# Kernel optimization log

Measured on AMD Instinct MI355X. Metric: run time of the kernel, lower is better.

## Reference

```python
import jax, jax.numpy as jnp
import numpy as np

DIM = 1024
HEADS = 16
HEAD_DIM = DIM // HEADS
SCALE = DIM ** (-0.5)  # NOTE: module scales by full dim, not head dim


def setup_inputs() -> dict:
    key = jax.random.key(0)
    k1, k2, k3, k4 = jax.random.split(key, 4)
    x = jax.random.normal(k1, (4, 2048, DIM), dtype=jnp.float32)
    w_qkv = jax.random.normal(k2, (DIM, 3 * DIM), dtype=jnp.float32) * (DIM ** -0.5)
    w_out = jax.random.normal(k3, (DIM, DIM), dtype=jnp.float32) * (DIM ** -0.5)
    b_out = jax.random.normal(k4, (DIM,), dtype=jnp.float32) * 0.01
    return {"x": x, "w_qkv": w_qkv, "w_out": w_out, "b_out": b_out}


def reference(x, w_qkv, w_out, b_out):
    b, n, _ = x.shape
    qkv = x @ w_qkv  # [b, n, 3*dim]
    # 'b n (qkv h d) -> qkv b h n d'
    qkv = qkv.reshape(b, n, 3, HEADS, HEAD_DIM).transpose(2, 0, 3, 1, 4)
    q, k, v = qkv[0], qkv[1], qkv[2]  # each [b, h, n, d]
    dots = jnp.einsum('bhid,bhjd->bhij', q, k) * SCALE
    attn = jax.nn.softmax(dots, axis=-1)
    out = jnp.einsum('bhij,bhjd->bhid', attn, v)
    out = out.transpose(0, 2, 1, 3).reshape(b, n, DIM)  # 'b h n d -> b n (h d)'
    return out @ w_out + b_out
```

## Files before the change

### kernel.cpp

```cpp
#include <hip/hip_runtime.h>
#include <math.h>

#define BATCH 4
#define SEQ   2048
#define DMODEL 1024
#define HEADS 16
#define DHEAD 64
#define SCALE 0.03125f
#define KEXP  0.045084220027780106f
#define QKV_ELEMS (BATCH * HEADS * SEQ * DHEAD)

typedef __attribute__((ext_vector_type(8))) short short8;
typedef __attribute__((ext_vector_type(4))) float floatx4;
typedef unsigned int u32;

__device__ __forceinline__ unsigned short f2bf(float f) {
  union { float f; unsigned u; } v;
  v.f = f;
  return (unsigned short)((v.u + 0x7FFFu + ((v.u >> 16) & 1u)) >> 16);
}

__device__ __forceinline__ float fast_exp2(float x) {
#if __has_builtin(__builtin_amdgcn_exp2f)
  return __builtin_amdgcn_exp2f(x);
#else
  return __expf(x * 0.6931471805599453f);
#endif
}

__device__ __forceinline__ u32 pack_bf16(float p0, float p1) {
#if __has_builtin(__builtin_amdgcn_cvt_pk_bf16_f32)
  typedef __bf16 bf16x2 __attribute__((ext_vector_type(2)));
  bf16x2 t = __builtin_amdgcn_cvt_pk_bf16_f32(p0, p1);
  u32 r;
  __builtin_memcpy(&r, &t, 4);
  return r;
#else
  u32 a0 = __float_as_uint(p0) + 0x8000u;
  u32 a1 = __float_as_uint(p1) + 0x8000u;
  return __builtin_amdgcn_perm(a1, a0, 0x07060302);
#endif
}

__device__ __forceinline__ void async_ld16(const void* g, void* l) {
  __builtin_amdgcn_global_load_lds(
      (const __attribute__((address_space(1))) u32*)g,
      (__attribute__((address_space(3))) u32*)l, 16, 0, 0);
}

__device__ __forceinline__ void trans_tile(const float* __restrict__ W,
                                           unsigned short* __restrict__ WT,
                                           int K, int N, int n0, int k0,
                                           float (*tile)[33]) {
  const int tx = threadIdx.x & 31, ty = threadIdx.x >> 5;
#pragma unroll
  for (int i = 0; i < 4; ++i)
    tile[ty + i * 8][tx] = W[(size_t)(k0 + ty + i * 8) * N + n0 + tx];
  __syncthreads();
#pragma unroll
  for (int i = 0; i < 4; ++i)
    WT[(size_t)(n0 + ty + i * 8) * K + k0 + tx] = f2bf(tile[tx][ty + i * 8]);
}

__global__ __launch_bounds__(256) void prep_kernel(
    const float* __restrict__ x, const float* __restrict__ wqkv,
    const float* __restrict__ wout, unsigned short* __restrict__ xb,
    unsigned short* __restrict__ wqkvT, unsigned short* __restrict__ woutT) {
  __shared__ float tile[32][33];
  const int bx = blockIdx.x;
  if (bx < 8192) {
    size_t i = ((size_t)bx * 256 + threadIdx.x) * 4;
    float4 v = *(const float4*)(x + i);
    ushort4 o;
    o.x = f2bf(v.x); o.y = f2bf(v.y); o.z = f2bf(v.z); o.w = f2bf(v.w);
    *(ushort4*)(xb + i) = o;
  } else if (bx < 11264) {
    int t = bx - 8192;
    trans_tile(wqkv, wqkvT, 1024, 3072, (t % 96) * 32, (t / 96) * 32, tile);
  } else {
    int t = bx - 11264;
    trans_tile(wout, woutT, 1024, 1024, (t % 32) * 32, (t / 32) * 32, tile);
  }
}

__device__ __forceinline__ void gemm_core(
    const unsigned short* __restrict__ A, const unsigned short* __restrict__ BT,
    unsigned short* As, unsigned short* Bs, int m0, int n0,
    floatx4 acc[4][4]) {
  const int tid = threadIdx.x;
  const int wave = tid >> 6, lane = tid & 63;
  const int quad = lane >> 4, l16 = lane & 15;
  const int wm = wave >> 1, wn = wave & 1;
  const int lrow = lane >> 3, ls = lane & 7;
  const int dblk = ls ^ (lrow & 7);
  const int sw = l16 & 7;

#pragma unroll
  for (int mt = 0; mt < 4; ++mt)
#pragma unroll
    for (int nt = 0; nt < 4; ++nt) acc[mt][nt] = (floatx4){0.f, 0.f, 0.f, 0.f};

  for (int k0 = 0; k0 < DMODEL; k0 += 64) {
    __syncthreads();
#pragma unroll
    for (int i = 0; i < 4; ++i) {
      int chunk = wave * 4 + i;
      int row = chunk * 8 + lrow;
      async_ld16(A + (size_t)(m0 + row) * DMODEL + k0 + dblk * 8,
                 As + chunk * 512);
      async_ld16(BT + (size_t)(n0 + row) * DMODEL + k0 + dblk * 8,
                 Bs + chunk * 512);
    }
    __syncthreads();
#pragma unroll
    for (int kk = 0; kk < 64; kk += 32) {
      const int kb = kk >> 3;
      short8 a[4], b[4];
#pragma unroll
      for (int t = 0; t < 4; ++t) {
        int row = wm * 64 + t * 16 + l16;
        a[t] = *(short8*)(As + row * 64 + (((kb + quad) ^ sw) * 8));
        int rowb = wn * 64 + t * 16 + l16;
        b[t] = *(short8*)(Bs + rowb * 64 + (((kb + quad) ^ sw) * 8));
      }
#pragma unroll
      for (int mt = 0; mt < 4; ++mt)
#pragma unroll
        for (int nt = 0; nt < 4; ++nt)
          acc[mt][nt] = __builtin_amdgcn_mfma_f32_16x16x32_bf16(
              a[mt], b[nt], acc[mt][nt], 0, 0, 0);
    }
  }
}

__global__ __launch_bounds__(256) void gemm_qkv_kernel(
    const unsigned short* __restrict__ A, const unsigned short* __restrict__ BT,
    unsigned short* __restrict__ qk, unsigned short* __restrict__ vtg) {
  __shared__ __align__(16) unsigned char smem[128 * 136 * 2];
  unsigned short* As = (unsigned short*)smem;
  unsigned short* Bs = As + 128 * 64;
  unsigned short* T = (unsigned short*)smem;
  const int tid = threadIdx.x;
  const int wave = tid >> 6, lane = tid & 63;
  const int quad = lane >> 4, l16 = lane & 15;
  const int wm = wave >> 1, wn = wave & 1;
  const int m0 = blockIdx.y * 128, n0 = blockIdx.x * 128;
  floatx4 acc[4][4];
  gemm_core(A, BT, As, Bs, m0, n0, acc);

  const int b = m0 >> 11, ntok = m0 & 2047;
  __syncthreads();

  if (blockIdx.x < 16) {
    const float qsc = (blockIdx.x < 8) ? KEXP : 1.0f;
#pragma unroll
    for (int mt = 0; mt < 4; ++mt) {
#pragma unroll
      for (int nt = 0; nt < 4; ++nt) {
        int c = wn * 64 + nt * 16 + l16;
#pragma unroll
        for (int r = 0; r < 4; ++r) {
          int mloc = wm * 64 + mt * 16 + quad * 4 + r;
          T[mloc * 132 + c] = f2bf(acc[mt][nt][r] * qsc);
        }
      }
    }
    __syncthreads();
    const int which = blockIdx.x >> 3;
    const int h0 = (n0 >> 6) & 15;
    const int inner = tid & 7;
#pragma unroll
    for (int pass = 0; pass < 8; ++pass) {
      int row = pass * 32 + (tid >> 3);
      int token = row >> 1, hh = row & 1;
      *(short8*)(qk + (size_t)which * QKV_ELEMS +
                 (((size_t)((b * HEADS + h0 + hh) * SEQ + ntok + token)) << 6) +
                 inner * 8) = *(short8*)&T[token * 132 + hh * 64 + inner * 8];
    }
  } else {
#pragma unroll
    for (int mt = 0; mt < 4; ++mt) {
#pragma unroll
      for (int nt = 0; nt < 4; ++nt) {
        int c = wn * 64 + nt * 16 + l16;
#pragma unroll
        for (int r = 0; r < 4; ++r) {
          int mloc = wm * 64 + mt * 16 + quad * 4 + r;
          int pcm = (mloc & ~31) | ((mloc & 15) << 1) | ((mloc >> 4) & 1);
          T[c * 136 + pcm] = f2bf(acc[mt][nt][r]);
        }
      }
    }
    __syncthreads();
    const int c = tid >> 1, hh = tid & 1;
    const int nc = n0 - 2048 + c;
    const int h = nc >> 6, d = nc & 63;
    const size_t dstbase =
        (((size_t)(b * HEADS + h)) * DHEAD + d) * SEQ + ntok;
#pragma unroll
    for (int j = 0; j < 8; ++j) {
      int t0 = (2 * j + hh) * 8;
      *(short8*)(vtg + dstbase + t0) = *(short8*)&T[c * 136 + t0];
    }
  }
}

__global__ __launch_bounds__(256) void gemm_out_kernel(
    const unsigned short* __restrict__ A, const unsigned short* __restrict__ BT,
    const float* __restrict__ bias, float* __restrict__ C) {
  __shared__ __align__(16) unsigned short As[128 * 64];
  __shared__ __align__(16) unsigned short Bs[128 * 64];
  const int tid = threadIdx.x;
  const int wave = tid >> 6, lane = tid & 63;
  const int quad = lane >> 4, l16 = lane & 15;
  const int wm = wave >> 1, wn = wave & 1;
  const int m0 = blockIdx.y * 128, n0 = blockIdx.x * 128;
  floatx4 acc[4][4];
  gemm_core(A, BT, As, Bs, m0, n0, acc);

#pragma unroll
  for (int mt = 0; mt < 4; ++mt) {
#pragma unroll
    for (int nt = 0; nt < 4; ++nt) {
      int nc = n0 + wn * 64 + nt * 16 + l16;
      float bv = bias[nc];
#pragma unroll
      for (int r = 0; r < 4; ++r) {
        int m = m0 + wm * 64 + mt * 16 + quad * 4 + r;
        C[(size_t)m * DMODEL + nc] = acc[mt][nt][r] + bv;
      }
    }
  }
}

__global__ __launch_bounds__(256, 4) void attn_kernel(
    const unsigned short* __restrict__ Qb, const unsigned short* __restrict__ Kb,
    const unsigned short* __restrict__ Vtg, unsigned short* __restrict__ Op) {
  __shared__ __align__(16) unsigned short Ks[2][64 * 64];
  __shared__ __align__(16) unsigned short Vs[2][64 * 64];
  __shared__ __align__(16) unsigned short Pl[4][16][40];
  const int tid = threadIdx.x;
  const int wave = tid >> 6, lane = tid & 63;
  const int quad = lane >> 4, l16 = lane & 15;
  const int bh = blockIdx.x & 63, qt = blockIdx.x >> 6;
  const size_t base = (size_t)bh * SEQ * DHEAD;
  const int lrow = lane >> 3, ls = lane & 7;
  const int dblk = ls ^ (lrow & 7);
  const int sw = l16 & 7;

  const unsigned short* kbase = Kb + base;
  const unsigned short* vbase = Vtg + base;
  const int c0 = wave * 2, c1 = wave * 2 + 1;
  const int row0 = c0 * 8 + lrow, row1 = c1 * 8 + lrow;

  short8 onesf;
#pragma unroll
  for (int i = 0; i < 8; ++i) onesf[i] = (short)0x3F80;

  short8 qf[2][2];
#pragma unroll
  for (int qs = 0; qs < 2; ++qs) {
    int qrow = qt * 128 + wave * 32 + qs * 16 + l16;
    qf[qs][0] = *(const short8*)(Qb + base + (size_t)qrow * DHEAD + quad * 8);
    qf[qs][1] =
        *(const short8*)(Qb + base + (size_t)qrow * DHEAD + 32 + quad * 8);
  }

  floatx4 o[2][4], lacc[2];
#pragma unroll
  for (int qs = 0; qs < 2; ++qs) {
    lacc[qs] = (floatx4){0.f, 0.f, 0.f, 0.f};
#pragma unroll
    for (int dt = 0; dt < 4; ++dt) o[qs][dt] = (floatx4){0.f, 0.f, 0.f, 0.f};
  }

#define STAGE(buf, kc)                                                         \
  do {                                                                         \
    async_ld16(kbase + (size_t)((kc)*64 + row0) * DHEAD + dblk * 8,            \
               &Ks[buf][c0 * 512]);                                            \
    async_ld16(vbase + (size_t)row0 * SEQ + (kc)*64 + dblk * 8,                \
               &Vs[buf][c0 * 512]);                                            \
    async_ld16(kbase + (size_t)((kc)*64 + row1) * DHEAD + dblk * 8,            \
               &Ks[buf][c1 * 512]);                                            \
    async_ld16(vbase + (size_t)row1 * SEQ + (kc)*64 + dblk * 8,                \
               &Vs[buf][c1 * 512]);                                            \
  } while (0)

#define COMPUTE(buf)                                                           \
  do {                                                                         \
    _Pragma("unroll") for (int kc2 = 0; kc2 < 2; ++kc2) {                      \
      const int krow = kc2 * 32;                                               \
      short8 kf00 =                                                            \
          *(short8*)(&Ks[buf][0] + (krow + l16) * 64 + ((quad ^ sw) * 8));     \
      short8 kf01 = *(short8*)(&Ks[buf][0] + (krow + l16) * 64 +               \
                               (((4 + quad) ^ sw) * 8));                       \
      short8 kf10 = *(short8*)(&Ks[buf][0] + (krow + 16 + l16) * 64 +          \
                               ((quad ^ sw) * 8));                             \
      short8 kf11 = *(short8*)(&Ks[buf][0] + (krow + 16 + l16) * 64 +          \
                               (((4 + quad) ^ sw) * 8));                       \
      short8 vf[4];                                                            \
      _Pragma("unroll") for (int dt = 0; dt < 4; ++dt) vf[dt] =                \
          *(short8*)(&Vs[buf][0] + (dt * 16 + l16) * 64 +                      \
                     (((kc2 * 4 + quad) ^ sw) * 8));                           \
      _Pragma("unroll") for (int qs = 0; qs < 2; ++qs) {                       \
        floatx4 s0 = (floatx4){0.f, 0.f, 0.f, 0.f};                            \
        floatx4 s1 = (floatx4){0.f, 0.f, 0.f, 0.f};                            \
        s0 = __builtin_amdgcn_mfma_f32_16x16x32_bf16(qf[qs][0], kf00, s0, 0,   \
                                                     0, 0);                    \
        s0 = __builtin_amdgcn_mfma_f32_16x16x32_bf16(qf[qs][1], kf01, s0, 0,   \
                                                     0, 0);                    \
        s1 = __builtin_amdgcn_mfma_f32_16x16x32_bf16(qf[qs][0], kf10, s1, 0,   \
                                                     0, 0);                    \
        s1 = __builtin_amdgcn_mfma_f32_16x16x32_bf16(qf[qs][1], kf11, s1, 0,   \
                                                     0, 0);                    \
        _Pragma("unroll") for (int r = 0; r < 4; ++r) {                        \
          float p0 = fast_exp2(s0[r]);                                         \
          float p1 = fast_exp2(s1[r]);                                         \
          *(u32*)&Pl[wave][quad * 4 + r][2 * l16] = pack_bf16(p0, p1);         \
        }                                                                      \
        short8 pf = *(short8*)&Pl[wave][l16][quad * 8];                        \
        lacc[qs] = __builtin_amdgcn_mfma_f32_16x16x32_bf16(pf, onesf,          \
                                                           lacc[qs], 0, 0, 0); \
        _Pragma("unroll") for (int dt = 0; dt < 4; ++dt) o[qs][dt] =           \
            __builtin_amdgcn_mfma_f32_16x16x32_bf16(pf, vf[dt], o[qs][dt], 0,  \
                                                    0, 0);                     \
      }                                                                        \
    }                                                                          \
  } while (0)

  STAGE(0, 0);
  for (int kc = 0; kc < SEQ / 64; kc += 2) {
    __syncthreads();
    if (kc + 1 < SEQ / 64) STAGE(1, kc + 1);
    COMPUTE(0);
    __syncthreads();
    if (kc + 2 < SEQ / 64) STAGE(0, kc + 2);
    COMPUTE(1);
  }
#undef STAGE
#undef COMPUTE

  const int b = bh >> 4, h = bh & 15;
#pragma unroll
  for (int qs = 0; qs < 2; ++qs) {
#pragma unroll
    for (int r = 0; r < 4; ++r) {
      float inv = 1.f / lacc[qs][r];
      int n = qt * 128 + wave * 32 + qs * 16 + quad * 4 + r;
      size_t rowbase = ((size_t)(b * SEQ + n)) * DMODEL + h * DHEAD;
#pragma unroll
      for (int dt = 0; dt < 4; ++dt)
        Op[rowbase + dt * 16 + l16] = f2bf(o[qs][dt][r] * inv);
    }
  }
}

extern "C" void kernel_launch(void* const* d_in, const int* in_sizes, int n_in,
                              void* d_out, int out_size, void* d_ws,
                              size_t ws_size, hipStream_t stream) {
  const float* x = (const float*)d_in[0];
  const float* w_qkv = (const float*)d_in[1];
  const float* w_out = (const float*)d_in[2];
  const float* b_out = (const float*)d_in[3];
  float* out = (float*)d_out;

  unsigned short* ws = (unsigned short*)d_ws;
  unsigned short* xb = ws;
  unsigned short* wqkvT = xb + 8388608;
  unsigned short* woutT = wqkvT + 3145728;
  unsigned short* qb = woutT + 1048576;
  unsigned short* kb = qb + QKV_ELEMS;
  unsigned short* vtg = kb + QKV_ELEMS;
  unsigned short* op = vtg + QKV_ELEMS;

  prep_kernel<<<dim3(12288), dim3(256), 0, stream>>>(x, w_qkv, w_out, xb,
                                                     wqkvT, woutT);
  gemm_qkv_kernel<<<dim3(24, 64), dim3(256), 0, stream>>>(xb, wqkvT, qb, vtg);
  attn_kernel<<<dim3(1024), dim3(256), 0, stream>>>(qb, kb, vtg, op);
  gemm_out_kernel<<<dim3(8, 64), dim3(256), 0, stream>>>(op, woutT, b_out, out);
}
```

Before: 270.5 us.

## Replace QKV GEMM with 256x256-tile, 8-wave, double-buffered async-load kernel

```diff
diff --git a/kernel.cpp b/kernel.cpp
--- a/kernel.cpp
+++ b/kernel.cpp
@@ -133,77 +133,212 @@
   }
 }
 
-__global__ __launch_bounds__(256) void gemm_qkv_kernel(
+#define BAR() __builtin_amdgcn_s_barrier()
+#define LGKM0() asm volatile("s_waitcnt lgkmcnt(0)" ::: "memory")
+
+#define STAGE_HALF(Gp, growbase, kcol, ldsh)                                   \
+  do {                                                                         \
+    async_ld16((Gp) + (size_t)((growbase) + srow) * 1024 + (kcol) +            \
+                   schunk * 8,                                                 \
+               (ldsh) + tid * 8);                                              \
+    async_ld16((Gp) + (size_t)((growbase) + 64 + srow) * 1024 + (kcol) +       \
+                   schunk * 8,                                                 \
+               (ldsh) + 4096 + tid * 8);                                       \
+  } while (0)
+
+#define RD_A(SAp, mh)                                                          \
+  do {                                                                         \
+    _Pragma("unroll") for (int mi = 0; mi < 4; ++mi) {                         \
+      _Pragma("unroll") for (int kh = 0; kh < 2; ++kh) {                       \
+        a[mi][kh] = *(const short8*)((SAp) + rowA + ((mh)*4 + mi) * 1024 +     \
+                                     cof[kh]);                                 \
+      }                                                                        \
+    }                                                                          \
+  } while (0)
+
+#define RD_B(SBp, nb)                                                          \
+  do {                                                                         \
+    _Pragma("unroll") for (int ni = 0; ni < 2; ++ni) {                         \
+      _Pragma("unroll") for (int kh = 0; kh < 2; ++kh) {                       \
+        b[(nb) + ni][kh] = *(const short8*)((SBp) + rowB +                     \
+                                            ((nb) + ni) * 1024 + cof[kh]);     \
+      }                                                                        \
+    }                                                                          \
+  } while (0)
+
+#define CLUSTER(mh, nb)                                                        \
+  do {                                                                         \
+    __builtin_amdgcn_s_setprio(1);                                             \
+    _Pragma("unroll") for (int mi = 0; mi < 4; ++mi) {                         \
+      _Pragma("unroll") for (int ni = 0; ni < 2; ++ni) {                       \
+        _Pragma("unroll") for (int kh = 0; kh < 2; ++kh) {                     \
+          acc[(mh)*4 + mi][(nb) + ni] =                                        \
+              __builtin_amdgcn_mfma_f32_16x16x32_bf16(                         \
+                  a[mi][kh], b[(nb) + ni][kh], acc[(mh)*4 + mi][(nb) + ni],    \
+                  0, 0, 0);                                                    \
+        }                                                                      \
+      }                                                                        \
+    }                                                                          \
+    __builtin_amdgcn_s_setprio(0);                                             \
+  } while (0)
+
+__global__ __launch_bounds__(512, 2) void gemm_qkv256_kernel(
     const unsigned short* __restrict__ A, const unsigned short* __restrict__ BT,
     unsigned short* __restrict__ qk, unsigned short* __restrict__ vtg) {
-  __shared__ __align__(16) unsigned char smem[128 * 136 * 2];
-  unsigned short* As = (unsigned short*)smem;
-  unsigned short* Bs = As + 128 * 64;
+  __shared__ __align__(16) unsigned char smem[131072];
+  unsigned short* const SA0 = (unsigned short*)smem;
+  unsigned short* const SB0 = SA0 + 16384;
+  unsigned short* const SA1 = SA0 + 32768;
+  unsigned short* const SB1 = SA0 + 49152;
+
+  const int tid = threadIdx.x;
+  const int wave = tid >> 6;
+  const int lane = tid & 63;
+  const int Q4 = lane >> 4, L = lane & 15;
+  const int wr = wave >> 2;
+  const int wc = wave & 3;
+
+  const int flat = blockIdx.y * 12 + blockIdx.x;
+  const int swz = (flat & 7) * 48 + (flat >> 3);
+  const int mblk = swz / 12, nblk = swz % 12;
+  const int m0 = mblk * 256, n0 = nblk * 256;
+
+  const int srow = tid >> 3;
+  const int schunk = (tid & 7) ^ (srow & 7);
+
+  const int xorL = L & 7;
+  const int cof[2] = {(Q4 ^ xorL) * 8, ((4 + Q4) ^ xorL) * 8};
+  const int rowA = wr * 8192 + L * 64;
+  const int rowB = wc * 4096 + L * 64;
+
+  short8 a[4][2], b[4][2];
+  floatx4 acc[8][4];
+#pragma unroll
+  for (int mt = 0; mt < 8; ++mt)
+#pragma unroll
+    for (int nt = 0; nt < 4; ++nt) acc[mt][nt] = (floatx4){0.f, 0.f, 0.f, 0.f};
+
+  STAGE_HALF(BT, n0, 0, SB0);
+  STAGE_HALF(BT, n0 + 128, 0, SB0 + 8192);
+  STAGE_HALF(A, m0, 0, SA0);
+  STAGE_HALF(A, m0 + 128, 0, SA0 + 8192);
+  STAGE_HALF(BT, n0, 64, SB1);
+  STAGE_HALF(BT, n0 + 128, 64, SB1 + 8192);
+  STAGE_HALF(A, m0, 64, SA1);
+  asm volatile("s_waitcnt vmcnt(6)" ::: "memory");
+  BAR();
+
+  for (int it = 0; it < 8; ++it) {
+    const int kt0 = it * 128, kt1 = kt0 + 64;
+    const bool pf = (it < 7);
+    RD_A(SA0, 0); RD_B(SB0, 0);
+    STAGE_HALF(A, m0 + 128, kt1, SA1 + 8192);
+    BAR(); LGKM0(); CLUSTER(0, 0); BAR();
+    RD_B(SB0, 2);
+    BAR(); LGKM0(); CLUSTER(0, 2); BAR();
+    RD_A(SA0, 1);
+    if (pf) {
+      STAGE_HALF(BT, n0, kt0 + 128, SB0);
+      STAGE_HALF(BT, n0 + 128, kt0 + 128, SB0 + 8192);
+    }
+    BAR(); LGKM0(); CLUSTER(1, 2); BAR();
+    if (pf) STAGE_HALF(A, m0, kt0 + 128, SA0);
+    BAR(); LGKM0(); CLUSTER(1, 0);
+    if (pf) asm volatile("s_waitcnt vmcnt(6)" ::: "memory");
+    else    asm volatile("s_waitcnt vmcnt(0)" ::: "memory");
+    BAR();
+    RD_A(SA1, 0); RD_B(SB1, 0);
+    if (pf) STAGE_HALF(A, m0 + 128, kt0 + 128, SA0 + 8192);
+    BAR(); LGKM0(); CLUSTER(0, 0); BAR();
+    RD_B(SB1, 2);
+    BAR(); LGKM0(); CLUSTER(0, 2); BAR();
+    RD_A(SA1, 1);
+    if (pf) {
+      STAGE_HALF(BT, n0, kt1 + 128, SB1);
+      STAGE_HALF(BT, n0 + 128, kt1 + 128, SB1 + 8192);
+    }
+    BAR(); LGKM0(); CLUSTER(1, 2); BAR();
+    if (pf) STAGE_HALF(A, m0, kt1 + 128, SA1);
+    BAR(); LGKM0(); CLUSTER(1, 0);
+    asm volatile("s_waitcnt vmcnt(6)" ::: "memory");
+    BAR();
+  }
+
+  const int bb = m0 >> 11;
+  const int ntok0 = m0 & 2047;
   unsigned short* T = (unsigned short*)smem;
-  const int tid = threadIdx.x;
-  const int wave = tid >> 6, lane = tid & 63;
-  const int quad = lane >> 4, l16 = lane & 15;
-  const int wm = wave >> 1, wn = wave & 1;
-  const int m0 = blockIdx.y * 128, n0 = blockIdx.x * 128;
-  floatx4 acc[4][4];
-  gemm_core(A, BT, As, Bs, m0, n0, acc);
-
-  const int b = m0 >> 11, ntok = m0 & 2047;
-  __syncthreads();
-
-  if (blockIdx.x < 16) {
-    const float qsc = (blockIdx.x < 8) ? KEXP : 1.0f;
-#pragma unroll
-    for (int mt = 0; mt < 4; ++mt) {
-#pragma unroll
-      for (int nt = 0; nt < 4; ++nt) {
-        int c = wn * 64 + nt * 16 + l16;
-#pragma unroll
-        for (int r = 0; r < 4; ++r) {
-          int mloc = wm * 64 + mt * 16 + quad * 4 + r;
-          T[mloc * 132 + c] = f2bf(acc[mt][nt][r] * qsc);
-        }
+  const int r4 = Q4 * 4;
+
+  if (nblk < 8) {
+    const float qsc = (nblk < 4) ? KEXP : 1.0f;
+    unsigned short* dst = qk + (size_t)(nblk >> 2) * QKV_ELEMS;
+    const int h0 = (nblk & 3) * 4;
+#pragma unroll
+    for (int wrp = 0; wrp < 2; ++wrp) {
+      if (wr == wrp) {
+#pragma unroll
+        for (int mt = 0; mt < 8; ++mt)
+#pragma unroll
+          for (int nt = 0; nt < 4; ++nt) {
+            const int col = wc * 64 + nt * 16 + L;
+#pragma unroll
+            for (int r = 0; r < 4; ++r)
+              T[(mt * 16 + r4 + r) * 264 + col] = f2bf(acc[mt][nt][r] * qsc);
+          }
       }
-    }
-    __syncthreads();
-    const int which = blockIdx.x >> 3;
-    const int h0 = (n0 >> 6) & 15;
-    const int inner = tid & 7;
-#pragma unroll
-    for (int pass = 0; pass < 8; ++pass) {
-      int row = pass * 32 + (tid >> 3);
-      int token = row >> 1, hh = row & 1;
-      *(short8*)(qk + (size_t)which * QKV_ELEMS +
-                 (((size_t)((b * HEADS + h0 + hh) * SEQ + ntok + token)) << 6) +
-                 inner * 8) = *(short8*)&T[token * 132 + hh * 64 + inner * 8];
+      __syncthreads();
+#pragma unroll
+      for (int it2 = 0; it2 < 8; ++it2) {
+        int slot = it2 * 512 + tid;
+        int tok_l = slot >> 5, ch = slot & 31;
+        int hs = ch >> 3, inner = ch & 7;
+        *(short8*)(dst +
+                   (((size_t)((bb * 16 + h0 + hs) * 2048 + ntok0 + wrp * 128 +
+                              tok_l)) << 6) + inner * 8) =
+            *(const short8*)&T[tok_l * 264 + ch * 8];
+      }
+      __syncthreads();
     }
   } else {
-#pragma unroll
-    for (int mt = 0; mt < 4; ++mt) {
-#pragma unroll
-      for (int nt = 0; nt < 4; ++nt) {
-        int c = wn * 64 + nt * 16 + l16;
-#pragma unroll
-        for (int r = 0; r < 4; ++r) {
-          int mloc = wm * 64 + mt * 16 + quad * 4 + r;
-          int pcm = (mloc & ~31) | ((mloc & 15) << 1) | ((mloc >> 4) & 1);
-          T[c * 136 + pcm] = f2bf(acc[mt][nt][r]);
-        }
+    const int nv0 = (nblk - 8) * 256;
+#pragma unroll
+    for (int wcp = 0; wcp < 2; ++wcp) {
+      if ((wc >> 1) == wcp) {
+#pragma unroll
+        for (int mt = 0; mt < 8; ++mt)
+#pragma unroll
+          for (int nt = 0; nt < 4; ++nt) {
+            const int col_l = (wc & 1) * 64 + nt * 16 + L;
+#pragma unroll
+            for (int r = 0; r < 4; ++r) {
+              int tok_l = wr * 128 + mt * 16 + r4 + r;
+              int pcm =
+                  (tok_l & ~31) | ((tok_l & 15) << 1) | ((tok_l >> 4) & 1);
+              T[col_l * 264 + pcm] = f2bf(acc[mt][nt][r]);
+            }
+          }
       }
-    }
-    __syncthreads();
-    const int c = tid >> 1, hh = tid & 1;
-    const int nc = n0 - 2048 + c;
-    const int h = nc >> 6, d = nc & 63;
-    const size_t dstbase =
-        (((size_t)(b * HEADS + h)) * DHEAD + d) * SEQ + ntok;
-#pragma unroll
-    for (int j = 0; j < 8; ++j) {
-      int t0 = (2 * j + hh) * 8;
-      *(short8*)(vtg + dstbase + t0) = *(short8*)&T[c * 136 + t0];
-    }
-  }
-}
+      __syncthreads();
+#pragma unroll
+      for (int it2 = 0; it2 < 8; ++it2) {
+        int slot = it2 * 512 + tid;
+        int col_l = slot >> 5, ch = slot & 31;
+        int nc = nv0 + wcp * 128 + col_l;
+        *(short8*)(vtg +
+                   (((size_t)((bb * 16 + (nc >> 6)) * 64 + (nc & 63))) << 11) +
+                   ntok0 + ch * 8) = *(const short8*)&T[col_l * 264 + ch * 8];
+      }
+      __syncthreads();
+    }
+  }
+}
+
+#undef STAGE_HALF
+#undef RD_A
+#undef RD_B
+#undef CLUSTER
+#undef BAR
+#undef LGKM0
 
 __global__ __launch_bounds__(256) void gemm_out_kernel(
     const unsigned short* __restrict__ A, const unsigned short* __restrict__ BT,
@@ -375,7 +510,8 @@
 
   prep_kernel<<<dim3(12288), dim3(256), 0, stream>>>(x, w_qkv, w_out, xb,
                                                      wqkvT, woutT);
-  gemm_qkv_kernel<<<dim3(24, 64), dim3(256), 0, stream>>>(xb, wqkvT, qb, vtg);
+  gemm_qkv256_kernel<<<dim3(12, 32), dim3(512), 0, stream>>>(xb, wqkvT, qb,
+                                                             vtg);
   attn_kernel<<<dim3(1024), dim3(256), 0, stream>>>(qb, kb, vtg, op);
   gemm_out_kernel<<<dim3(8, 64), dim3(256), 0, stream>>>(op, woutT, b_out, out);
 }
```

New measurement: 267.4 us. Within noise of the previous version (-1.1%).

## Rewrite GEMMs as 256x128 tiles with triple-buffered async LDS pipeline

Applied to the files above, without the earlier changes.

```diff
diff --git a/kernel.cpp b/kernel.cpp
--- a/kernel.cpp
+++ b/kernel.cpp
@@ -83,155 +83,213 @@
   }
 }
 
-__device__ __forceinline__ void gemm_core(
+#define G_BAR() __builtin_amdgcn_s_barrier()
+#define G_LGKM0() asm volatile("s_waitcnt lgkmcnt(0)" ::: "memory")
+
+#define STAGE_TILE(t)                                                          \
+  do {                                                                         \
+    const unsigned short* Ab =                                                 \
+        A + (size_t)(m0 + srow) * 1024 + (t) * 64 + schunk * 8;                \
+    const unsigned short* Bb =                                                 \
+        BT + (size_t)(n0 + srow) * 1024 + (t) * 64 + schunk * 8;               \
+    unsigned short* sa = smemS + ((t) % 3) * 24576;                            \
+    unsigned short* sb = sa + 16384;                                           \
+    async_ld16(Ab, sa + tid * 8);                                              \
+    async_ld16(Ab + 64 * 1024, sa + 4096 + tid * 8);                           \
+    async_ld16(Ab + 128 * 1024, sa + 8192 + tid * 8);                          \
+    async_ld16(Ab + 192 * 1024, sa + 12288 + tid * 8);                         \
+    async_ld16(Bb, sb + tid * 8);                                              \
+    async_ld16(Bb + 64 * 1024, sb + 4096 + tid * 8);                           \
+  } while (0)
+
+#define RD_A(SAp, mh)                                                          \
+  do {                                                                         \
+    _Pragma("unroll") for (int mi = 0; mi < 4; ++mi) {                         \
+      a[mi][0] = *(const short8*)((SAp) + rowA + (mh)*4096 + mi * 1024 + cof0);\
+      a[mi][1] = *(const short8*)((SAp) + rowA + (mh)*4096 + mi * 1024 + cof1);\
+    }                                                                          \
+  } while (0)
+
+#define RD_B(SBp)                                                              \
+  do {                                                                         \
+    _Pragma("unroll") for (int ni = 0; ni < 2; ++ni) {                         \
+      b[ni][0] = *(const short8*)((SBp) + rowB + ni * 1024 + cof0);            \
+      b[ni][1] = *(const short8*)((SBp) + rowB + ni * 1024 + cof1);            \
+    }                                                                          \
+  } while (0)
+
+#define CLUSTER(mh)                                                            \
+  do {                                                                         \
+    __builtin_amdgcn_s_setprio(1);                                             \
+    _Pragma("unroll") for (int mi = 0; mi < 4; ++mi) {                         \
+      _Pragma("unroll") for (int ni = 0; ni < 2; ++ni) {                       \
+        acc[(mh)*4 + mi][ni] = __builtin_amdgcn_mfma_f32_16x16x32_bf16(        \
+            a[mi][0], b[ni][0], acc[(mh)*4 + mi][ni], 0, 0, 0);                \
+        acc[(mh)*4 + mi][ni] = __builtin_amdgcn_mfma_f32_16x16x32_bf16(        \
+            a[mi][1], b[ni][1], acc[(mh)*4 + mi][ni], 0, 0, 0);                \
+      }                                                                        \
+    }                                                                          \
+    __builtin_amdgcn_s_setprio(0);                                             \
+  } while (0)
+
+__device__ __forceinline__ void core256x128(
     const unsigned short* __restrict__ A, const unsigned short* __restrict__ BT,
-    unsigned short* As, unsigned short* Bs, int m0, int n0,
-    floatx4 acc[4][4]) {
+    unsigned short* smemS, int m0, int n0, floatx4 (&acc)[8][2]) {
   const int tid = threadIdx.x;
   const int wave = tid >> 6, lane = tid & 63;
-  const int quad = lane >> 4, l16 = lane & 15;
-  const int wm = wave >> 1, wn = wave & 1;
-  const int lrow = lane >> 3, ls = lane & 7;
-  const int dblk = ls ^ (lrow & 7);
-  const int sw = l16 & 7;
-
-#pragma unroll
-  for (int mt = 0; mt < 4; ++mt)
-#pragma unroll
-    for (int nt = 0; nt < 4; ++nt) acc[mt][nt] = (floatx4){0.f, 0.f, 0.f, 0.f};
-
-  for (int k0 = 0; k0 < DMODEL; k0 += 64) {
-    __syncthreads();
-#pragma unroll
-    for (int i = 0; i < 4; ++i) {
-      int chunk = wave * 4 + i;
-      int row = chunk * 8 + lrow;
-      async_ld16(A + (size_t)(m0 + row) * DMODEL + k0 + dblk * 8,
-                 As + chunk * 512);
-      async_ld16(BT + (size_t)(n0 + row) * DMODEL + k0 + dblk * 8,
-                 Bs + chunk * 512);
-    }
-    __syncthreads();
-#pragma unroll
-    for (int kk = 0; kk < 64; kk += 32) {
-      const int kb = kk >> 3;
-      short8 a[4], b[4];
-#pragma unroll
-      for (int t = 0; t < 4; ++t) {
-        int row = wm * 64 + t * 16 + l16;
-        a[t] = *(short8*)(As + row * 64 + (((kb + quad) ^ sw) * 8));
-        int rowb = wn * 64 + t * 16 + l16;
-        b[t] = *(short8*)(Bs + rowb * 64 + (((kb + quad) ^ sw) * 8));
-      }
-#pragma unroll
-      for (int mt = 0; mt < 4; ++mt)
-#pragma unroll
-        for (int nt = 0; nt < 4; ++nt)
-          acc[mt][nt] = __builtin_amdgcn_mfma_f32_16x16x32_bf16(
-              a[mt], b[nt], acc[mt][nt], 0, 0, 0);
-    }
-  }
-}
-
-__global__ __launch_bounds__(256) void gemm_qkv_kernel(
+  const int Q4 = lane >> 4, L = lane & 15;
+  const int wr = wave >> 2, wc = wave & 3;
+  const int srow = tid >> 3;
+  const int schunk = (tid & 7) ^ (srow & 7);
+  const int xorL = L & 7;
+  const int cof0 = (Q4 ^ xorL) * 8;
+  const int cof1 = ((4 + Q4) ^ xorL) * 8;
+  const int rowA = wr * 8192 + L * 64;
+  const int rowB = wc * 2048 + L * 64;
+
+  short8 a[4][2], b[2][2];
+#pragma unroll
+  for (int mt = 0; mt < 8; ++mt)
+#pragma unroll
+    for (int nt = 0; nt < 2; ++nt) acc[mt][nt] = (floatx4){0.f, 0.f, 0.f, 0.f};
+
+  STAGE_TILE(0);
+  STAGE_TILE(1);
+  asm volatile("s_waitcnt vmcnt(6)" ::: "memory");
+  G_BAR();
+
+#pragma unroll
+  for (int u = 0; u < 16; ++u) {
+    unsigned short* SA = smemS + (u % 3) * 24576;
+    unsigned short* SB = SA + 16384;
+    RD_A(SA, 0);
+    RD_B(SB);
+    if (u + 2 < 16) STAGE_TILE(u + 2);
+    G_BAR(); G_LGKM0();
+    CLUSTER(0);
+    G_BAR();
+    RD_A(SA, 1);
+    G_BAR(); G_LGKM0();
+    CLUSTER(1);
+    if (u + 2 < 16) asm volatile("s_waitcnt vmcnt(6)" ::: "memory");
+    else            asm volatile("s_waitcnt vmcnt(0)" ::: "memory");
+    G_BAR();
+  }
+}
+
+__global__ __launch_bounds__(512, 2) void gemm_qkv_kernel(
     const unsigned short* __restrict__ A, const unsigned short* __restrict__ BT,
     unsigned short* __restrict__ qk, unsigned short* __restrict__ vtg) {
-  __shared__ __align__(16) unsigned char smem[128 * 136 * 2];
-  unsigned short* As = (unsigned short*)smem;
-  unsigned short* Bs = As + 128 * 64;
-  unsigned short* T = (unsigned short*)smem;
+  __shared__ __align__(16) unsigned char smem[147456];
+  unsigned short* smemS = (unsigned short*)smem;
+
   const int tid = threadIdx.x;
   const int wave = tid >> 6, lane = tid & 63;
-  const int quad = lane >> 4, l16 = lane & 15;
-  const int wm = wave >> 1, wn = wave & 1;
-  const int m0 = blockIdx.y * 128, n0 = blockIdx.x * 128;
-  floatx4 acc[4][4];
-  gemm_core(A, BT, As, Bs, m0, n0, acc);
-
-  const int b = m0 >> 11, ntok = m0 & 2047;
-  __syncthreads();
-
-  if (blockIdx.x < 16) {
-    const float qsc = (blockIdx.x < 8) ? KEXP : 1.0f;
-#pragma unroll
-    for (int mt = 0; mt < 4; ++mt) {
-#pragma unroll
-      for (int nt = 0; nt < 4; ++nt) {
-        int c = wn * 64 + nt * 16 + l16;
+  const int Q4 = lane >> 4, L = lane & 15;
+  const int wr = wave >> 2, wc = wave & 3;
+
+  const int flat = blockIdx.y * 24 + blockIdx.x;
+  const int swz = (flat & 7) * 96 + (flat >> 3);
+  const int mblk = swz / 24, nblk = swz % 24;
+  const int m0 = mblk * 256, n0 = nblk * 128;
+
+  floatx4 acc[8][2];
+  core256x128(A, BT, smemS, m0, n0, acc);
+
+  const int bb = m0 >> 11;
+  const int ntok0 = m0 & 2047;
+  unsigned short* T = smemS;
+
+  if (nblk < 16) {
+    const float qsc = (nblk < 8) ? KEXP : 1.0f;
+    unsigned short* dst = qk + (size_t)(nblk >> 3) * QKV_ELEMS;
+    const int h0 = (nblk & 7) * 2;
+#pragma unroll
+    for (int mt = 0; mt < 8; ++mt)
+#pragma unroll
+      for (int nt = 0; nt < 2; ++nt) {
+        const int col = wc * 32 + nt * 16 + L;
+        const int tokl = wr * 128 + mt * 16 + Q4 * 4;
+#pragma unroll
+        for (int r = 0; r < 4; ++r)
+          T[(tokl + r) * 136 + col] = f2bf(acc[mt][nt][r] * qsc);
+      }
+    __syncthreads();
+#pragma unroll
+    for (int it2 = 0; it2 < 8; ++it2) {
+      int slot = it2 * 512 + tid;
+      int tok = slot >> 4, ch = slot & 15;
+      int hh = ch >> 3, inner = ch & 7;
+      *(short8*)(dst +
+                 (((size_t)((bb * 16 + h0 + hh) * 2048 + ntok0 + tok)) << 6) +
+                 inner * 8) = *(const short8*)&T[tok * 136 + hh * 64 + inner * 8];
+    }
+  } else {
+    const int nv0 = (nblk - 16) * 128;
+#pragma unroll
+    for (int mt = 0; mt < 8; ++mt)
+#pragma unroll
+      for (int nt = 0; nt < 2; ++nt) {
+        const int col = wc * 32 + nt * 16 + L;
 #pragma unroll
         for (int r = 0; r < 4; ++r) {
-          int mloc = wm * 64 + mt * 16 + quad * 4 + r;
-          T[mloc * 132 + c] = f2bf(acc[mt][nt][r] * qsc);
+          int tok = wr * 128 + mt * 16 + Q4 * 4 + r;
+          int pcm = (tok & ~31) | ((tok & 15) << 1) | ((tok >> 4) & 1);
+          T[col * 264 + pcm] = f2bf(acc[mt][nt][r]);
         }
       }
+    __syncthreads();
+#pragma unroll
+    for (int it2 = 0; it2 < 8; ++it2) {
+      int slot = it2 * 512 + tid;
+      int col = slot >> 5, ch = slot & 31;
+      int nc = nv0 + col;
+      *(short8*)(vtg +
+                 (((size_t)((bb * 16 + (nc >> 6)) * 64 + (nc & 63))) << 11) +
+                 ntok0 + ch * 8) = *(const short8*)&T[col * 264 + ch * 8];
     }
-    __syncthreads();
-    const int which = blockIdx.x >> 3;
-    const int h0 = (n0 >> 6) & 15;
-    const int inner = tid & 7;
-#pragma unroll
-    for (int pass = 0; pass < 8; ++pass) {
-      int row = pass * 32 + (tid >> 3);
-      int token = row >> 1, hh = row & 1;
-      *(short8*)(qk + (size_t)which * QKV_ELEMS +
-                 (((size_t)((b * HEADS + h0 + hh) * SEQ + ntok + token)) << 6) +
-                 inner * 8) = *(short8*)&T[token * 132 + hh * 64 + inner * 8];
-    }
-  } else {
-#pragma unroll
-    for (int mt = 0; mt < 4; ++mt) {
-#pragma unroll
-      for (int nt = 0; nt < 4; ++nt) {
-        int c = wn * 64 + nt * 16 + l16;
-#pragma unroll
-        for (int r = 0; r < 4; ++r) {
-          int mloc = wm * 64 + mt * 16 + quad * 4 + r;
-          int pcm = (mloc & ~31) | ((mloc & 15) << 1) | ((mloc >> 4) & 1);
-          T[c * 136 + pcm] = f2bf(acc[mt][nt][r]);
-        }
-      }
-    }
-    __syncthreads();
-    const int c = tid >> 1, hh = tid & 1;
-    const int nc = n0 - 2048 + c;
-    const int h = nc >> 6, d = nc & 63;
-    const size_t dstbase =
-        (((size_t)(b * HEADS + h)) * DHEAD + d) * SEQ + ntok;
-#pragma unroll
-    for (int j = 0; j < 8; ++j) {
-      int t0 = (2 * j + hh) * 8;
-      *(short8*)(vtg + dstbase + t0) = *(short8*)&T[c * 136 + t0];
-    }
-  }
-}
-
-__global__ __launch_bounds__(256) void gemm_out_kernel(
+  }
+}
+
+__global__ __launch_bounds__(512, 2) void gemm_out_kernel(
     const unsigned short* __restrict__ A, const unsigned short* __restrict__ BT,
     const float* __restrict__ bias, float* __restrict__ C) {
-  __shared__ __align__(16) unsigned short As[128 * 64];
-  __shared__ __align__(16) unsigned short Bs[128 * 64];
+  __shared__ __align__(16) unsigned char smem[147456];
+  unsigned short* smemS = (unsigned short*)smem;
+
   const int tid = threadIdx.x;
   const int wave = tid >> 6, lane = tid & 63;
-  const int quad = lane >> 4, l16 = lane & 15;
-  const int wm = wave >> 1, wn = wave & 1;
-  const int m0 = blockIdx.y * 128, n0 = blockIdx.x * 128;
-  floatx4 acc[4][4];
-  gemm_core(A, BT, As, Bs, m0, n0, acc);
-
-#pragma unroll
-  for (int mt = 0; mt < 4; ++mt) {
-#pragma unroll
-    for (int nt = 0; nt < 4; ++nt) {
-      int nc = n0 + wn * 64 + nt * 16 + l16;
+  const int Q4 = lane >> 4, L = lane & 15;
+  const int wr = wave >> 2, wc = wave & 3;
+
+  const int flat = blockIdx.y * 8 + blockIdx.x;
+  const int swz = (flat & 7) * 32 + (flat >> 3);
+  const int m0 = (swz >> 3) * 256, n0 = (swz & 7) * 128;
+
+  floatx4 acc[8][2];
+  core256x128(A, BT, smemS, m0, n0, acc);
+
+#pragma unroll
+  for (int mt = 0; mt < 8; ++mt) {
+#pragma unroll
+    for (int nt = 0; nt < 2; ++nt) {
+      int nc = n0 + wc * 32 + nt * 16 + L;
       float bv = bias[nc];
 #pragma unroll
       for (int r = 0; r < 4; ++r) {
-        int m = m0 + wm * 64 + mt * 16 + quad * 4 + r;
+        int m = m0 + wr * 128 + mt * 16 + Q4 * 4 + r;
         C[(size_t)m * DMODEL + nc] = acc[mt][nt][r] + bv;
       }
     }
   }
 }
+
+#undef STAGE_TILE
+#undef RD_A
+#undef RD_B
+#undef CLUSTER
+#undef G_BAR
+#undef G_LGKM0
 
 __global__ __launch_bounds__(256, 4) void attn_kernel(
     const unsigned short* __restrict__ Qb, const unsigned short* __restrict__ Kb,
@@ -375,7 +433,7 @@
 
   prep_kernel<<<dim3(12288), dim3(256), 0, stream>>>(x, w_qkv, w_out, xb,
                                                      wqkvT, woutT);
-  gemm_qkv_kernel<<<dim3(24, 64), dim3(256), 0, stream>>>(xb, wqkvT, qb, vtg);
+  gemm_qkv_kernel<<<dim3(24, 32), dim3(512), 0, stream>>>(xb, wqkvT, qb, vtg);
   attn_kernel<<<dim3(1024), dim3(256), 0, stream>>>(qb, kb, vtg, op);
-  gemm_out_kernel<<<dim3(8, 64), dim3(256), 0, stream>>>(op, woutT, b_out, out);
-}
+  gemm_out_kernel<<<dim3(8, 32), dim3(512), 0, stream>>>(op, woutT, b_out, out);
+}
```

New measurement: 256.2 us. 5.3% less time.
